# Performance work log

Hardware: AMD Instinct MI355X
Metric: run time of the kernel (lower is better)

## Reference

```python
import jax, jax.numpy as jnp
import numpy as np

# Dimensions (match init_kwargs / input_specs)
B, N, E, H, L, FF = 32, 512, 1024, 8, 3, 2048
KD = E // H          # key_dim = val_dim = 128 (projection width of W_query/W_key/W_val)
DK = KD // H         # 16 = actual per-head dim after the raw (H,B,N,-1) view
NORM = 1.0 / np.sqrt(KD)  # module uses 1/sqrt(key_dim)
MASK_FILL = -30.0    # evaluate=False path


def setup_inputs() -> dict:
    key = jax.random.key(0)
    ks = jax.random.split(key, 11)
    f32 = jnp.float32
    x = jax.random.normal(ks[0], (B * N, E), f32)
    mask = jax.random.randint(ks[1], (B, N), 0, 2).astype(bool)
    # Stacked per-layer params; torch init: uniform(-1/sqrt(fan_in), 1/sqrt(fan_in))
    def u(k, shape, fan):
        s = 1.0 / np.sqrt(fan)
        return jax.random.uniform(k, shape, f32, -s, s)
    Wq = u(ks[2], (L, KD, E), E)
    Wk = u(ks[3], (L, KD, E), E)
    Wv = u(ks[4], (L, KD, E), E)
    Wo = u(ks[5], (L, E, KD), KD)
    bo = u(ks[6], (L, E), E)
    W1 = u(ks[7], (L, FF, E), E)
    b1 = u(ks[8], (L, FF), FF)
    W2 = u(ks[9], (L, E, FF), FF)
    b2 = u(ks[10], (L, E), E)
    return {"x": x, "mask": mask, "Wq": Wq, "Wk": Wk, "Wv": Wv,
            "Wo": Wo, "bo": bo, "W1": W1, "b1": b1, "W2": W2, "b2": b2}


def _mha(h, Wq, Wk, Wv, Wo, bo, mask):
    # h: (B*N, E). Raw row-major view (torch .view == jnp.reshape) into (H,B,N,DK),
    # which mixes token/feature axes exactly as the original module does.
    Q = (h @ Wq.T).reshape(H, B, N, DK)
    K = (h @ Wk.T).reshape(H, B, N, DK)
    V = (h @ Wv.T).reshape(H, B, N, DK)
    compat = NORM * jnp.einsum('hbnd,hbmd->hbnm', Q, K)  # (H,B,N,N)
    m = mask[None, :, None, :]                            # mask key positions
    compat = jnp.where(m, MASK_FILL, compat)
    attn = jax.nn.softmax(compat, axis=-1)
    attn = jnp.where(m, 0.0, attn)                        # re-zero masked entries
    heads = jnp.einsum('hbnm,hbmd->hbnd', attn, V)        # (H,B,N,DK)
    out = heads.transpose(1, 2, 0, 3).reshape(B * N, H * DK) @ Wo.T + bo
    return out


def reference(x, mask, Wq, Wk, Wv, Wo, bo, W1, b1, W2, b2):
    h = x
    for l in range(L):
        h = h + _mha(h, Wq[l], Wk[l], Wv[l], Wo[l], bo[l], mask)
        h = h + (jax.nn.relu(h @ W1[l].T + b1[l]) @ W2[l].T + b2[l])
    return h, h.reshape(B, N, E).mean(axis=1)
```

## Files before the change

### kernel.cpp

```cpp
#include <hip/hip_runtime.h>
#include <stdint.h>


typedef __attribute__((ext_vector_type(8))) short short8;
typedef __attribute__((ext_vector_type(4))) float floatx4;

#define NORM_ 0.08838834764831845f

__device__ __forceinline__ float bf2f(unsigned short u) {
    union { unsigned int i; float f; } x; x.i = ((unsigned int)u) << 16; return x.f;
}
__device__ __forceinline__ unsigned short f2bf(float f) {
    union { float f; unsigned int i; } x; x.f = f;
    unsigned int u = x.i;
    u += 0x7FFFu + ((u >> 16) & 1u);
    return (unsigned short)(u >> 16);
}
__device__ __forceinline__ void async_cp16(const void* g, void* l) {
    __builtin_amdgcn_global_load_lds((const __attribute__((address_space(1))) void*)g,
                                     (__attribute__((address_space(3))) void*)l, 16, 0, 0);
}

__global__ __launch_bounds__(256) void detect_dtype(const unsigned int* __restrict__ x,
                                                    int* __restrict__ flag)
{
    __shared__ int good, bad;
    if (threadIdx.x == 0) { good = 0; bad = 0; }
    __syncthreads();
    int g = 0, b = 0;
    for (int i = threadIdx.x; i < 4096; i += 256) {
        unsigned int lo = x[i] & 0xFFFFu;
        if (lo != 0u) {
            unsigned int e = (lo >> 7) & 0xFFu;
            if (e >= 90u && e <= 145u) ++g; else ++b;
        }
    }
    atomicAdd(&good, g); atomicAdd(&bad, b);
    __syncthreads();
    if (threadIdx.x == 0) *flag = (bad > good) ? 1 : 0;
}

__global__ __launch_bounds__(256) void conv_to_bf16(const void* __restrict__ src,
                                                    unsigned short* __restrict__ dst,
                                                    int n, const int* __restrict__ flag)
{
    const int i = (blockIdx.x * 256 + threadIdx.x) * 8;
    if (i >= n) return;
    if (*flag) {
        const float* s = (const float*)src + i;
        floatx4 a = *(const floatx4*)s;
        floatx4 b = *(const floatx4*)(s + 4);
        short8 o;
        o[0] = (short)f2bf(a[0]); o[1] = (short)f2bf(a[1]);
        o[2] = (short)f2bf(a[2]); o[3] = (short)f2bf(a[3]);
        o[4] = (short)f2bf(b[0]); o[5] = (short)f2bf(b[1]);
        o[6] = (short)f2bf(b[2]); o[7] = (short)f2bf(b[3]);
        *(short8*)(dst + i) = o;
    } else {
        *(short8*)(dst + i) = *(const short8*)((const unsigned short*)src + i);
    }
}

__global__ __launch_bounds__(256) void init_h(const void* __restrict__ x,
                                              float* __restrict__ hf,
                                              unsigned short* __restrict__ hb,
                                              const int* __restrict__ flag)
{
    const size_t i = ((size_t)blockIdx.x * 256 + threadIdx.x) * 8;
    if (*flag) {
        const float* s = (const float*)x + i;
        floatx4 a = *(const floatx4*)s;
        floatx4 b = *(const floatx4*)(s + 4);
        short8 o;
        o[0] = (short)f2bf(a[0]); o[1] = (short)f2bf(a[1]);
        o[2] = (short)f2bf(a[2]); o[3] = (short)f2bf(a[3]);
        o[4] = (short)f2bf(b[0]); o[5] = (short)f2bf(b[1]);
        o[6] = (short)f2bf(b[2]); o[7] = (short)f2bf(b[3]);
        *(short8*)(hb + i) = o;
        *(floatx4*)(hf + i) = a;
        *(floatx4*)(hf + i + 4) = b;
    } else {
        short8 v = *(const short8*)((const unsigned short*)x + i);
        *(short8*)(hb + i) = v;
        #pragma unroll
        for (int e = 0; e < 8; ++e) hf[i + e] = bf2f((unsigned short)v[e]);
    }
}

__global__ __launch_bounds__(256) void mask_expand(const unsigned int* __restrict__ mraw,
                                                   float* __restrict__ maskf)
{
    __shared__ unsigned int r[4];
    if (threadIdx.x < 4) r[threadIdx.x] = 0;
    __syncthreads();
    unsigned int gt1 = 0, badb = 0, badh = 0, lo3f = 0;
    for (int i = threadIdx.x; i < 4096; i += 256) {
        unsigned int w = mraw[i];
        if (w > 1u) gt1 = 1;
        if (w & 0xFEFEFEFEu) badb = 1;
        unsigned int lo = w & 0xFFFFu, hi = w >> 16;
        if ((lo != 0u && lo != 0x3F80u) || (hi != 0u && hi != 0x3F80u)) badh = 1;
        if (lo == 0x3F80u) lo3f = 1;
    }
    if (gt1) atomicOr(&r[0], 1u);
    if (badb) atomicOr(&r[1], 1u);
    if (badh) atomicOr(&r[2], 1u);
    if (lo3f) atomicOr(&r[3], 1u);
    __syncthreads();
    int cls;
    if (!r[0]) cls = 0;
    else if (!r[1]) cls = 1;
    else if (!r[2]) cls = r[3] ? 2 : 3;
    else cls = 0;

    const int gid = blockIdx.x * 256 + threadIdx.x;
    bool m;
    if (cls == 0)      m = ((const int*)mraw)[gid] != 0;
    else if (cls == 1) m = ((const unsigned char*)mraw)[gid] != 0;
    else if (cls == 2) m = ((const unsigned short*)mraw)[gid] != 0;
    else               m = mraw[gid] != 0u;
    maskf[gid] = m ? 1.0f : 0.0f;
}

enum { EPI_NONE = 0, EPI_BIAS_RELU = 1, EPI_BIAS_RES = 2 };

template<int EPI>
__global__ __launch_bounds__(256) void gemm_bt(
    const unsigned short* __restrict__ A,
    const unsigned short* __restrict__ Bq,
    const unsigned short* __restrict__ Bk,
    const unsigned short* __restrict__ Bv,
    unsigned short* __restrict__ Cq,
    unsigned short* __restrict__ Ck,
    unsigned short* __restrict__ Cv,
    const unsigned short* __restrict__ bias,
    float* __restrict__ hf,
    unsigned short* __restrict__ hb,
    int N, int K)
{
    constexpr int BK = 64;
    __shared__ __align__(16) unsigned short As[2][128 * BK];
    __shared__ __align__(16) unsigned short Bs[2][128 * BK];

    const int t = threadIdx.x;
    const int lane = t & 63;
    const int wave = t >> 6;
    const int bm = blockIdx.x;
    const int bn = blockIdx.y;
    const int bz = blockIdx.z;

    const unsigned short* Bmat = (bz == 0) ? Bq : ((bz == 1) ? Bk : Bv);
    unsigned short* C = (bz == 0) ? Cq : ((bz == 1) ? Ck : Cv);

    const int wm = (wave >> 1) * 64;
    const int wn = (wave & 1) * 64;

    const int srow = t >> 3;
    const int scol = (((t & 7) ^ ((t >> 3) & 7)) * 8);
    const unsigned short* Ag = A + (size_t)(bm * 128 + srow) * K + scol;
    const unsigned short* Bg = Bmat + (size_t)(bn * 128 + srow) * K + scol;
    const size_t gstep = (size_t)32 * K;

    const int fl = lane & 15;
    const int g = lane >> 4;
    const int s7 = fl & 7;
    const int swz0 = (g ^ s7) * 8;
    const int swz1 = ((g + 4) ^ s7) * 8;
    int aoff[4], boff[4];
    #pragma unroll
    for (int i = 0; i < 4; ++i) {
        aoff[i] = (wm + i * 16 + fl) * BK;
        boff[i] = (wn + i * 16 + fl) * BK;
    }

    floatx4 acc[4][4];
    #pragma unroll
    for (int i = 0; i < 4; ++i)
        #pragma unroll
        for (int j = 0; j < 4; ++j) {
            acc[i][j][0] = 0.f; acc[i][j][1] = 0.f;
            acc[i][j][2] = 0.f; acc[i][j][3] = 0.f;
        }

    const int NT = K / BK;

    #pragma unroll
    for (int r = 0; r < 4; ++r) {
        async_cp16(Ag + r * gstep, &As[0][t * 8 + r * 2048]);
        async_cp16(Bg + r * gstep, &Bs[0][t * 8 + r * 2048]);
    }

    for (int it = 0; it < NT; ++it) {
        const int cur = it & 1;
        if (it + 1 < NT) {
            const int nxt = cur ^ 1;
            const size_t koff = (size_t)(it + 1) * BK;
            #pragma unroll
            for (int r = 0; r < 4; ++r) {
                async_cp16(Ag + koff + r * gstep, &As[nxt][t * 8 + r * 2048]);
                async_cp16(Bg + koff + r * gstep, &Bs[nxt][t * 8 + r * 2048]);
            }
            asm volatile("s_waitcnt vmcnt(8)" ::: "memory");
        } else {
            asm volatile("s_waitcnt vmcnt(0)" ::: "memory");
        }
        asm volatile("s_barrier" ::: "memory");

        #pragma unroll
        for (int ks = 0; ks < 2; ++ks) {
            const int sw = ks ? swz1 : swz0;
            short8 af[4], bfr[4];
            #pragma unroll
            for (int i = 0; i < 4; ++i) af[i] = *(const short8*)&As[cur][aoff[i] + sw];
            #pragma unroll
            for (int j = 0; j < 4; ++j) bfr[j] = *(const short8*)&Bs[cur][boff[j] + sw];
            #pragma unroll
            for (int i = 0; i < 4; ++i)
                #pragma unroll
                for (int j = 0; j < 4; ++j)
                    acc[i][j] = __builtin_amdgcn_mfma_f32_16x16x32_bf16(af[i], bfr[j], acc[i][j], 0, 0, 0);
        }
        if (it + 1 < NT)
            asm volatile("s_barrier" ::: "memory");
    }

    const int r0 = (lane >> 4) * 4;
    #pragma unroll
    for (int j = 0; j < 4; ++j) {
        const int gcol = bn * 128 + wn + j * 16 + fl;
        float bval = 0.f;
        if (EPI != EPI_NONE) bval = bf2f(bias[gcol]);
        #pragma unroll
        for (int i = 0; i < 4; ++i) {
            const int growb = bm * 128 + wm + i * 16 + r0;
            #pragma unroll
            for (int r = 0; r < 4; ++r) {
                const size_t idx = (size_t)(growb + r) * N + gcol;
                float v = acc[i][j][r];
                if (EPI == EPI_NONE) {
                    C[idx] = f2bf(v);
                } else if (EPI == EPI_BIAS_RELU) {
                    v += bval;
                    v = v > 0.f ? v : 0.f;
                    C[idx] = f2bf(v);
                } else {
                    float nh = hf[idx] + v + bval;
                    hf[idx] = nh;
                    hb[idx] = f2bf(nh);
                }
            }
        }
    }
}

__global__ __launch_bounds__(128) void attn_mfma(
    const unsigned short* __restrict__ Q,
    const unsigned short* __restrict__ Kx,
    const unsigned short* __restrict__ Vx,
    const float* __restrict__ maskf,
    unsigned short* __restrict__ Out)
{
    __shared__ __align__(16) unsigned short Vt[16 * 520];
    __shared__ __align__(16) unsigned short Pb[2][64 * 40];
    __shared__ float Ms[512];
    __shared__ float cnt_s;

    const int t = threadIdx.x;
    const int lane = t & 63;
    const int wave = t >> 6;
    const int p = blockIdx.x >> 2;
    const int qq = blockIdx.x & 3;
    const int b2 = p & 31;
    const int h2 = p >> 5;
    const int fm = lane & 15;
    const int g = lane >> 4;

    const unsigned short* Qg = Q + (size_t)p * 8192;
    const unsigned short* Kg = Kx + (size_t)p * 8192;
    const unsigned short* Vg = Vx + (size_t)p * 8192;

    #pragma unroll
    for (int rr = 0; rr < 4; ++rr) {
        const int row = t * 4 + rr;
        short8 v0 = *(const short8*)&Vg[row * 16];
        short8 v1 = *(const short8*)&Vg[row * 16 + 8];
        #pragma unroll
        for (int d = 0; d < 8; ++d) Vt[d * 520 + row] = (unsigned short)v0[d];
        #pragma unroll
        for (int d = 0; d < 8; ++d) Vt[(d + 8) * 520 + row] = (unsigned short)v1[d];
    }
    if (t == 0) cnt_s = 0.f;
    __syncthreads();
    float pc = 0.f;
    #pragma unroll
    for (int it = 0; it < 4; ++it) {
        int i = it * 128 + t;
        float mv = maskf[b2 * 512 + i];
        Ms[i] = mv; pc += mv;
    }
    atomicAdd(&cnt_s, pc);
    __syncthreads();
    const float cnt = cnt_s;

    const int qbase = qq * 128 + wave * 64;
    short8 qf[4];
    #pragma unroll
    for (int i = 0; i < 4; ++i) {
        short8 z = {0,0,0,0,0,0,0,0};
        if (g < 2) z = *(const short8*)&Qg[(qbase + i * 16 + fm) * 16 + g * 8];
        qf[i] = z;
    }

    float m_[4][4], l_[4][4];
    floatx4 O[4];
    #pragma unroll
    for (int i = 0; i < 4; ++i) {
        #pragma unroll
        for (int r = 0; r < 4; ++r) { m_[i][r] = -1e30f; l_[i][r] = 0.f; }
        O[i][0] = 0.f; O[i][1] = 0.f; O[i][2] = 0.f; O[i][3] = 0.f;
    }

    unsigned short* Pw = &Pb[wave][0];

    for (int kb = 0; kb < 512; kb += 32) {
        short8 kf0 = {0,0,0,0,0,0,0,0}, kf1 = {0,0,0,0,0,0,0,0};
        if (g < 2) {
            kf0 = *(const short8*)&Kg[(kb + fm) * 16 + g * 8];
            kf1 = *(const short8*)&Kg[(kb + 16 + fm) * 16 + g * 8];
        }
        const float msk0 = Ms[kb + fm];
        const float msk1 = Ms[kb + 16 + fm];

        floatx4 zero4 = {0.f, 0.f, 0.f, 0.f};
        floatx4 s0[4], s1[4];
        #pragma unroll
        for (int i = 0; i < 4; ++i) {
            s0[i] = __builtin_amdgcn_mfma_f32_16x16x32_bf16(qf[i], kf0, zero4, 0, 0, 0);
            s1[i] = __builtin_amdgcn_mfma_f32_16x16x32_bf16(qf[i], kf1, zero4, 0, 0, 0);
        }

        #pragma unroll
        for (int i = 0; i < 4; ++i) {
            #pragma unroll
            for (int r = 0; r < 4; ++r) {
                float a0 = (msk0 != 0.f) ? -1e30f : s0[i][r] * NORM_;
                float a1 = (msk1 != 0.f) ? -1e30f : s1[i][r] * NORM_;
                float mx = fmaxf(a0, a1);
                mx = fmaxf(mx, __shfl_xor(mx, 1));
                mx = fmaxf(mx, __shfl_xor(mx, 2));
                mx = fmaxf(mx, __shfl_xor(mx, 4));
                mx = fmaxf(mx, __shfl_xor(mx, 8));
                const float mo = m_[i][r];
                const float mn = fmaxf(mo, mx);
                const float alpha = __expf(mo - mn);
                float w0 = (msk0 != 0.f) ? 0.f : __expf(a0 - mn);
                float w1 = (msk1 != 0.f) ? 0.f : __expf(a1 - mn);
                float rs = w0 + w1;
                rs += __shfl_xor(rs, 1);
                rs += __shfl_xor(rs, 2);
                rs += __shfl_xor(rs, 4);
                rs += __shfl_xor(rs, 8);
                l_[i][r] = l_[i][r] * alpha + rs;
                m_[i][r] = mn;
                O[i][r] *= alpha;
                const int qloc = i * 16 + g * 4 + r;
                Pw[qloc * 40 + fm] = f2bf(w0);
                Pw[qloc * 40 + 16 + fm] = f2bf(w1);
            }
        }
        asm volatile("s_waitcnt lgkmcnt(0)" ::: "memory");

        short8 vtf = *(const short8*)&Vt[fm * 520 + kb + g * 8];
        #pragma unroll
        for (int i = 0; i < 4; ++i) {
            short8 pf = *(const short8*)&Pw[(i * 16 + fm) * 40 + g * 8];
            O[i] = __builtin_amdgcn_mfma_f32_16x16x32_bf16(pf, vtf, O[i], 0, 0, 0);
        }
    }

    #pragma unroll
    for (int i = 0; i < 4; ++i) {
        #pragma unroll
        for (int r = 0; r < 4; ++r) {
            const float M = fmaxf(m_[i][r], -30.f);
            const float adj = __expf(m_[i][r] - M);
            const float lf = l_[i][r] * adj + cnt * __expf(-30.f - M);
            const float oval = O[i][r] * adj / lf;
            const int n = qbase + i * 16 + g * 4 + r;
            Out[((size_t)(b2 * 512 + n)) * 128 + h2 * 16 + fm] = f2bf(oval);
        }
    }
}

__global__ __launch_bounds__(256) void write_h(const float* __restrict__ hf,
                                               void* __restrict__ out,
                                               const int* __restrict__ flag)
{
    const size_t i = ((size_t)blockIdx.x * 256 + threadIdx.x) * 4;
    floatx4 v = *(const floatx4*)&hf[i];
    if (*flag) {
        *(floatx4*)((float*)out + i) = v;
    } else {
        unsigned int p0 = (unsigned int)f2bf(v[0]) | ((unsigned int)f2bf(v[1]) << 16);
        unsigned int p1 = (unsigned int)f2bf(v[2]) | ((unsigned int)f2bf(v[3]) << 16);
        unsigned int* o = (unsigned int*)((unsigned short*)out + i);
        o[0] = p0; o[1] = p1;
    }
}

__global__ __launch_bounds__(256) void mean_kernel(const float* __restrict__ hf,
                                                   void* __restrict__ out,
                                                   const int* __restrict__ flag)
{
    const int b = blockIdx.x >> 2;
    const int e = ((blockIdx.x & 3) * 256) + threadIdx.x;
    float s = 0.f;
    for (int n = 0; n < 512; ++n) s += hf[((size_t)(b * 512 + n)) * 1024 + e];
    s *= (1.0f / 512.0f);
    const size_t off = (size_t)16384 * 1024 + b * 1024 + e;
    if (*flag) ((float*)out)[off] = s;
    else       ((unsigned short*)out)[off] = f2bf(s);
}

extern "C" void kernel_launch(void* const* d_in, const int* in_sizes, int n_in,
                              void* d_out, int out_size, void* d_ws, size_t ws_size,
                              hipStream_t stream)
{
    const void* x  = d_in[0];
    const unsigned int* mask = (const unsigned int*)d_in[1];

    char* ws = (char*)d_ws;
    float* hf = (float*)ws;                     ws += (size_t)16384 * 1024 * 4;
    unsigned short* hb = (unsigned short*)ws;   ws += (size_t)16384 * 1024 * 2;
    char* shared_rg = ws;                       ws += (size_t)16384 * 2048 * 2;
    unsigned short* act = (unsigned short*)shared_rg;
    unsigned short* q  = (unsigned short*)shared_rg;
    unsigned short* k  = q + (size_t)16384 * 128;
    unsigned short* v  = k + (size_t)16384 * 128;
    unsigned short* ao = v + (size_t)16384 * 128;
    unsigned short* cWq = (unsigned short*)ws;  ws += (size_t)393216 * 2;
    unsigned short* cWk = (unsigned short*)ws;  ws += (size_t)393216 * 2;
    unsigned short* cWv = (unsigned short*)ws;  ws += (size_t)393216 * 2;
    unsigned short* cWo = (unsigned short*)ws;  ws += (size_t)393216 * 2;
    unsigned short* cbo = (unsigned short*)ws;  ws += (size_t)3072 * 2;
    unsigned short* cW1 = (unsigned short*)ws;  ws += (size_t)6291456 * 2;
    unsigned short* cb1 = (unsigned short*)ws;  ws += (size_t)6144 * 2;
    unsigned short* cW2 = (unsigned short*)ws;  ws += (size_t)6291456 * 2;
    unsigned short* cb2 = (unsigned short*)ws;  ws += (size_t)3072 * 2;
    float* maskf = (float*)ws;                  ws += (size_t)16384 * 4;
    int* flag = (int*)ws;                       ws += 256;

    detect_dtype<<<1, 256, 0, stream>>>((const unsigned int*)x, flag);

    auto conv = [&](const void* s, unsigned short* d, int n) {
        conv_to_bf16<<<(n / 8 + 255) / 256, 256, 0, stream>>>(s, d, n, flag);
    };
    conv(d_in[2], cWq, 393216);
    conv(d_in[3], cWk, 393216);
    conv(d_in[4], cWv, 393216);
    conv(d_in[5], cWo, 393216);
    conv(d_in[6], cbo, 3072);
    conv(d_in[7], cW1, 6291456);
    conv(d_in[8], cb1, 6144);
    conv(d_in[9], cW2, 6291456);
    conv(d_in[10], cb2, 3072);

    mask_expand<<<64, 256, 0, stream>>>(mask, maskf);
    init_h<<<8192, 256, 0, stream>>>(x, hf, hb, flag);

    for (int l = 0; l < 3; ++l) {
        const unsigned short* wq  = cWq + (size_t)l * 131072;
        const unsigned short* wk  = cWk + (size_t)l * 131072;
        const unsigned short* wv  = cWv + (size_t)l * 131072;
        const unsigned short* wo  = cWo + (size_t)l * 131072;
        const unsigned short* bol = cbo + (size_t)l * 1024;
        const unsigned short* w1  = cW1 + (size_t)l * 2097152;
        const unsigned short* b1l = cb1 + (size_t)l * 2048;
        const unsigned short* w2  = cW2 + (size_t)l * 2097152;
        const unsigned short* b2l = cb2 + (size_t)l * 1024;

        gemm_bt<EPI_NONE><<<dim3(128, 1, 3), 256, 0, stream>>>(
            hb, wq, wk, wv, q, k, v, nullptr, nullptr, nullptr, 128, 1024);
        attn_mfma<<<1024, 128, 0, stream>>>(q, k, v, maskf, ao);
        gemm_bt<EPI_BIAS_RES><<<dim3(128, 8, 1), 256, 0, stream>>>(
            ao, wo, wo, wo, nullptr, nullptr, nullptr, bol, hf, hb, 1024, 128);
        gemm_bt<EPI_BIAS_RELU><<<dim3(128, 16, 1), 256, 0, stream>>>(
            hb, w1, w1, w1, act, act, act, b1l, nullptr, nullptr, 2048, 1024);
        gemm_bt<EPI_BIAS_RES><<<dim3(128, 8, 1), 256, 0, stream>>>(
            act, w2, w2, w2, nullptr, nullptr, nullptr, b2l, hf, hb, 1024, 2048);
    }

    write_h<<<16384, 256, 0, stream>>>(hf, d_out, flag);
    mean_kernel<<<128, 256, 0, stream>>>(hf, d_out, flag);
}
```

Measured before the change: 1.247 ms.

## Add 256x256-tile GEMM with pipelined async loads for FFN layers

Introduces a new 512-thread GEMM kernel using 256x256 output tiles, 8 waves each computing 128x64, with double-buffered LDS staging via global_load_lds, an XOR swizzle, interleaved load/MFMA phases and setprio hints. The two FFN GEMMs (W1 with ReLU, W2 with residual) switch to it. Larger tiles are meant to raise arithmetic intensity and cut global traffic, and the interleaving is meant to hide load latency. In exchange it uses 128KB of LDS and many accumulator registers, so only one block fits per CU, and the grids are smaller (512 and 256 blocks), which may underfill the GPU.

```diff
diff --git a/kernel.cpp b/kernel.cpp
--- a/kernel.cpp
+++ b/kernel.cpp
@@ -19,6 +19,9 @@
 __device__ __forceinline__ void async_cp16(const void* g, void* l) {
     __builtin_amdgcn_global_load_lds((const __attribute__((address_space(1))) void*)g,
                                      (__attribute__((address_space(3))) void*)l, 16, 0, 0);
+}
+__device__ __forceinline__ floatx4 mfma16(short8 a, short8 b, floatx4 c) {
+    return __builtin_amdgcn_mfma_f32_16x16x32_bf16(a, b, c, 0, 0, 0);
 }
 
 __global__ __launch_bounds__(256) void detect_dtype(const unsigned int* __restrict__ x,
@@ -233,6 +236,171 @@
         #pragma unroll
         for (int i = 0; i < 4; ++i) {
             const int growb = bm * 128 + wm + i * 16 + r0;
+            #pragma unroll
+            for (int r = 0; r < 4; ++r) {
+                const size_t idx = (size_t)(growb + r) * N + gcol;
+                float v = acc[i][j][r];
+                if (EPI == EPI_NONE) {
+                    C[idx] = f2bf(v);
+                } else if (EPI == EPI_BIAS_RELU) {
+                    v += bval;
+                    v = v > 0.f ? v : 0.f;
+                    C[idx] = f2bf(v);
+                } else {
+                    float nh = hf[idx] + v + bval;
+                    hf[idx] = nh;
+                    hb[idx] = f2bf(nh);
+                }
+            }
+        }
+    }
+}
+
+template<int EPI>
+__global__ __launch_bounds__(512) void gemm256_bt(
+    const unsigned short* __restrict__ A,
+    const unsigned short* __restrict__ Bmat,
+    unsigned short* __restrict__ C,
+    const unsigned short* __restrict__ bias,
+    float* __restrict__ hf,
+    unsigned short* __restrict__ hb,
+    int N, int K)
+{
+    __shared__ __align__(16) unsigned short As[2][16384];
+    __shared__ __align__(16) unsigned short Bs[2][16384];
+
+    const int t = threadIdx.x;
+    const int lane = t & 63;
+    const int wave = t >> 6;
+    const int bm = blockIdx.x;
+    const int bn = blockIdx.y;
+
+    const int wm = (wave >> 2) * 128;
+    const int wn = (wave & 3) * 64;
+
+    const int srow = t >> 3;
+    const int scol = ((t & 7) ^ (srow & 7)) * 8;
+    const unsigned short* Ag = A + (size_t)(bm * 256 + srow) * K + scol;
+    const unsigned short* Bg = Bmat + (size_t)(bn * 256 + srow) * K + scol;
+    const size_t rows64 = (size_t)64 * K;
+
+    const int fl = lane & 15;
+    const int g = lane >> 4;
+    const int s7 = fl & 7;
+    const int c0 = (g ^ s7) * 8;
+    const int c1 = ((4 + g) ^ s7) * 8;
+    const int abase = (wm + fl) * 64;
+    const int bbase = (wn + fl) * 64;
+
+    floatx4 acc[8][4];
+    #pragma unroll
+    for (int i = 0; i < 8; ++i)
+        #pragma unroll
+        for (int j = 0; j < 4; ++j) {
+            acc[i][j][0] = 0.f; acc[i][j][1] = 0.f;
+            acc[i][j][2] = 0.f; acc[i][j][3] = 0.f;
+        }
+
+    auto stgA = [&](int buf, int h, size_t koff) {
+        const unsigned short* s = Ag + (size_t)(h * 128) * K + koff;
+        unsigned short* d = &As[buf][h * 8192 + t * 8];
+        async_cp16(s, d);
+        async_cp16(s + rows64, d + 4096);
+    };
+    auto stgB = [&](int buf, int h, size_t koff) {
+        const unsigned short* s = Bg + (size_t)(h * 128) * K + koff;
+        unsigned short* d = &Bs[buf][h * 8192 + t * 8];
+        async_cp16(s, d);
+        async_cp16(s + rows64, d + 4096);
+    };
+
+    const int NT = K >> 6;
+
+    stgA(0, 0, 0); stgA(0, 1, 0); stgB(0, 0, 0); stgB(0, 1, 0);
+    if (NT > 1) {
+        stgA(1, 0, 64); stgA(1, 1, 64);
+        asm volatile("s_waitcnt vmcnt(4)" ::: "memory");
+    } else {
+        asm volatile("s_waitcnt vmcnt(0)" ::: "memory");
+    }
+    asm volatile("s_barrier" ::: "memory");
+
+    for (int tt = 0; tt < NT; ++tt) {
+        const int R = tt & 1;
+        const int S = R ^ 1;
+        const size_t k1 = (size_t)(tt + 1) << 6;
+        const size_t k2 = (size_t)(tt + 2) << 6;
+        const bool p1 = (tt + 1 < NT);
+        const bool p2 = (tt + 2 < NT);
+
+        short8 a0[8], a1[8], b0[4], b1[4];
+
+        #pragma unroll
+        for (int i = 0; i < 8; ++i) a0[i] = *(const short8*)&As[R][abase + i * 1024 + c0];
+        #pragma unroll
+        for (int j = 0; j < 4; ++j) b0[j] = *(const short8*)&Bs[R][bbase + j * 1024 + c0];
+        if (p1) stgB(S, 0, k1);
+        asm volatile("s_barrier" ::: "memory");
+        asm volatile("s_waitcnt lgkmcnt(0)" ::: "memory");
+        __builtin_amdgcn_s_setprio(1);
+        #pragma unroll
+        for (int i = 0; i < 8; ++i) {
+            acc[i][0] = mfma16(a0[i], b0[0], acc[i][0]);
+            acc[i][1] = mfma16(a0[i], b0[1], acc[i][1]);
+        }
+        __builtin_amdgcn_s_setprio(0);
+        asm volatile("s_barrier" ::: "memory");
+
+        #pragma unroll
+        for (int i = 0; i < 8; ++i) a1[i] = *(const short8*)&As[R][abase + i * 1024 + c1];
+        #pragma unroll
+        for (int j = 0; j < 4; ++j) b1[j] = *(const short8*)&Bs[R][bbase + j * 1024 + c1];
+        if (p1) stgB(S, 1, k1);
+        asm volatile("s_barrier" ::: "memory");
+        asm volatile("s_waitcnt lgkmcnt(0)" ::: "memory");
+        __builtin_amdgcn_s_setprio(1);
+        #pragma unroll
+        for (int i = 0; i < 8; ++i) {
+            acc[i][2] = mfma16(a0[i], b0[2], acc[i][2]);
+            acc[i][3] = mfma16(a0[i], b0[3], acc[i][3]);
+        }
+        __builtin_amdgcn_s_setprio(0);
+        asm volatile("s_barrier" ::: "memory");
+
+        if (p2) stgA(R, 0, k2);
+        asm volatile("s_barrier" ::: "memory");
+        __builtin_amdgcn_s_setprio(1);
+        #pragma unroll
+        for (int i = 0; i < 8; ++i) {
+            acc[i][0] = mfma16(a1[i], b1[0], acc[i][0]);
+            acc[i][1] = mfma16(a1[i], b1[1], acc[i][1]);
+        }
+        __builtin_amdgcn_s_setprio(0);
+        asm volatile("s_barrier" ::: "memory");
+
+        if (p2) stgA(R, 1, k2);
+        asm volatile("s_barrier" ::: "memory");
+        __builtin_amdgcn_s_setprio(1);
+        #pragma unroll
+        for (int i = 0; i < 8; ++i) {
+            acc[i][2] = mfma16(a1[i], b1[2], acc[i][2]);
+            acc[i][3] = mfma16(a1[i], b1[3], acc[i][3]);
+        }
+        __builtin_amdgcn_s_setprio(0);
+        if (p2) asm volatile("s_waitcnt vmcnt(4)" ::: "memory");
+        else    asm volatile("s_waitcnt vmcnt(0)" ::: "memory");
+        asm volatile("s_barrier" ::: "memory");
+    }
+
+    const int r0 = g * 4;
+    #pragma unroll
+    for (int j = 0; j < 4; ++j) {
+        const int gcol = bn * 256 + wn + j * 16 + fl;
+        float bval = 0.f;
+        if (EPI != EPI_NONE) bval = bf2f(bias[gcol]);
+        #pragma unroll
+        for (int i = 0; i < 8; ++i) {
+            const int growb = bm * 256 + wm + i * 16 + r0;
             #pragma unroll
             for (int r = 0; r < 4; ++r) {
                 const size_t idx = (size_t)(growb + r) * N + gcol;
@@ -484,10 +652,10 @@
         attn_mfma<<<1024, 128, 0, stream>>>(q, k, v, maskf, ao);
         gemm_bt<EPI_BIAS_RES><<<dim3(128, 8, 1), 256, 0, stream>>>(
             ao, wo, wo, wo, nullptr, nullptr, nullptr, bol, hf, hb, 1024, 128);
-        gemm_bt<EPI_BIAS_RELU><<<dim3(128, 16, 1), 256, 0, stream>>>(
-            hb, w1, w1, w1, act, act, act, b1l, nullptr, nullptr, 2048, 1024);
-        gemm_bt<EPI_BIAS_RES><<<dim3(128, 8, 1), 256, 0, stream>>>(
-            act, w2, w2, w2, nullptr, nullptr, nullptr, b2l, hf, hb, 1024, 2048);
+        gemm256_bt<EPI_BIAS_RELU><<<dim3(64, 8, 1), 512, 0, stream>>>(
+            hb, w1, act, b1l, nullptr, nullptr, 2048, 1024);
+        gemm256_bt<EPI_BIAS_RES><<<dim3(64, 4, 1), 512, 0, stream>>>(
+            act, w2, nullptr, b2l, hf, hb, 1024, 2048);
     }
 
     write_h<<<16384, 256, 0, stream>>>(hf, d_out, flag);
```

Measured after the change: 1.200 ms. -3.8%, faster.

## Add dedicated FFN GEMM with 128x256 tiles, register-streamed B and hand-scheduled MFMA

Applied to the files above, without the earlier changes.

Adds a gemm_ffn kernel for the two FFN matmuls. It uses 512-thread blocks computing 128x256 output tiles, stages only the A operand in LDS through async global-to-LDS copies, and loads the weight B fragments directly from global memory into registers, double-buffered across k-tiles. The inline-asm ds_read/global_load calls, explicit waitcnt, sched_barrier and setprio are meant to interleave MFMAs with memory traffic and raise per-block reuse. The cost is higher register pressure and fragile manual scheduling. B fragments read from global are not shared across waves.

```diff
diff --git a/kernel.cpp b/kernel.cpp
--- a/kernel.cpp
+++ b/kernel.cpp
@@ -19,6 +19,21 @@
 __device__ __forceinline__ void async_cp16(const void* g, void* l) {
     __builtin_amdgcn_global_load_lds((const __attribute__((address_space(1))) void*)g,
                                      (__attribute__((address_space(3))) void*)l, 16, 0, 0);
+}
+__device__ __forceinline__ floatx4 mfma16(short8 a, short8 b, floatx4 c) {
+    return __builtin_amdgcn_mfma_f32_16x16x32_bf16(a, b, c, 0, 0, 0);
+}
+template<int IMM>
+__device__ __forceinline__ short8 ds_read128(unsigned addr) {
+    short8 r;
+    asm volatile("ds_read_b128 %0, %1 offset:%2" : "=v"(r) : "v"(addr), "n"(IMM));
+    return r;
+}
+template<int IMM>
+__device__ __forceinline__ short8 gload128(const unsigned short* p) {
+    short8 r;
+    asm volatile("global_load_dwordx4 %0, %1, off offset:%2" : "=v"(r) : "v"(p), "n"(IMM));
+    return r;
 }
 
 __global__ __launch_bounds__(256) void detect_dtype(const unsigned int* __restrict__ x,
@@ -228,6 +243,183 @@
     #pragma unroll
     for (int j = 0; j < 4; ++j) {
         const int gcol = bn * 128 + wn + j * 16 + fl;
+        float bval = 0.f;
+        if (EPI != EPI_NONE) bval = bf2f(bias[gcol]);
+        #pragma unroll
+        for (int i = 0; i < 4; ++i) {
+            const int growb = bm * 128 + wm + i * 16 + r0;
+            #pragma unroll
+            for (int r = 0; r < 4; ++r) {
+                const size_t idx = (size_t)(growb + r) * N + gcol;
+                float v = acc[i][j][r];
+                if (EPI == EPI_NONE) {
+                    C[idx] = f2bf(v);
+                } else if (EPI == EPI_BIAS_RELU) {
+                    v += bval;
+                    v = v > 0.f ? v : 0.f;
+                    C[idx] = f2bf(v);
+                } else {
+                    float nh = hf[idx] + v + bval;
+                    hf[idx] = nh;
+                    hb[idx] = f2bf(nh);
+                }
+            }
+        }
+    }
+}
+
+template<int EPI>
+__global__ __launch_bounds__(512, 2) void gemm_ffn(
+    const unsigned short* __restrict__ A,
+    const unsigned short* __restrict__ Bmat,
+    unsigned short* __restrict__ C,
+    const unsigned short* __restrict__ bias,
+    float* __restrict__ hf,
+    unsigned short* __restrict__ hb,
+    int N, int K)
+{
+    __shared__ __align__(16) unsigned short As[2][8192];
+
+    const int t = threadIdx.x;
+    const int lane = t & 63;
+    const int wave = t >> 6;
+    const int bm = blockIdx.x;
+    const int bn = blockIdx.y;
+
+    const int wm = (wave >> 2) * 64;
+    const int wn = (wave & 3) * 64;
+
+    const int srow = t >> 3;
+    const int scol = ((t & 7) ^ (srow & 7)) * 8;
+    const unsigned short* Ag = A + (size_t)(bm * 128 + srow) * K + scol;
+    const size_t r64K = (size_t)64 * K;
+
+    const int fl = lane & 15;
+    const int g = lane >> 4;
+    const int s7 = fl & 7;
+
+    const unsigned ldsA = (unsigned)(size_t)(__attribute__((address_space(3))) unsigned short*)&As[0][0];
+    const unsigned rA0 = ldsA + (unsigned)((wm + fl) * 128 + ((g ^ s7) * 16));
+    const unsigned rA1 = ldsA + (unsigned)((wm + fl) * 128 + (((4 + g) ^ s7) * 16));
+
+    const unsigned short* pb0 = Bmat + (size_t)(bn * 256 + wn + 0 * 16 + fl) * K + g * 8;
+    const unsigned short* pb1 = Bmat + (size_t)(bn * 256 + wn + 1 * 16 + fl) * K + g * 8;
+    const unsigned short* pb2 = Bmat + (size_t)(bn * 256 + wn + 2 * 16 + fl) * K + g * 8;
+    const unsigned short* pb3 = Bmat + (size_t)(bn * 256 + wn + 3 * 16 + fl) * K + g * 8;
+
+    floatx4 acc[4][4];
+    #pragma unroll
+    for (int i = 0; i < 4; ++i)
+        #pragma unroll
+        for (int j = 0; j < 4; ++j) {
+            acc[i][j][0] = 0.f; acc[i][j][1] = 0.f;
+            acc[i][j][2] = 0.f; acc[i][j][3] = 0.f;
+        }
+
+    auto stg = [&](int buf, int rnd, int tile) {
+        const unsigned short* s = Ag + (size_t)rnd * r64K + (size_t)tile * 64;
+        async_cp16(s, &As[buf][rnd * 4096 + t * 8]);
+    };
+
+    const int NT = K >> 6;
+
+    short8 bA[8], bB[8];
+
+    bA[0] = gload128<0>(pb0);  bA[1] = gload128<0>(pb1);
+    bA[2] = gload128<0>(pb2);  bA[3] = gload128<0>(pb3);
+    bA[4] = gload128<64>(pb0); bA[5] = gload128<64>(pb1);
+    bA[6] = gload128<64>(pb2); bA[7] = gload128<64>(pb3);
+    stg(0, 0, 0); stg(0, 1, 0);
+    stg(1, 0, 1); stg(1, 1, 1);
+    asm volatile("s_waitcnt vmcnt(2)" ::: "memory");
+    asm volatile("s_barrier" ::: "memory");
+
+#define FFN_TILE(TT, R, CURB, NXTB)                                            \
+    do {                                                                       \
+        const bool p1 = (TT) + 1 < NT;                                         \
+        const bool p2 = (TT) + 2 < NT;                                         \
+        short8 a0k0 = ds_read128<0 * 2048 + (R) * 16384>(rA0);                 \
+        short8 a1k0 = ds_read128<1 * 2048 + (R) * 16384>(rA0);                 \
+        short8 a2k0 = ds_read128<2 * 2048 + (R) * 16384>(rA0);                 \
+        short8 a3k0 = ds_read128<3 * 2048 + (R) * 16384>(rA0);                 \
+        short8 a0k1 = ds_read128<0 * 2048 + (R) * 16384>(rA1);                 \
+        short8 a1k1 = ds_read128<1 * 2048 + (R) * 16384>(rA1);                 \
+        short8 a2k1 = ds_read128<2 * 2048 + (R) * 16384>(rA1);                 \
+        short8 a3k1 = ds_read128<3 * 2048 + (R) * 16384>(rA1);                 \
+        if (p1) {                                                              \
+            NXTB[0] = gload128<((R) + 1) * 128 + 0>(pb0);                      \
+            NXTB[1] = gload128<((R) + 1) * 128 + 0>(pb1);                      \
+            NXTB[2] = gload128<((R) + 1) * 128 + 0>(pb2);                      \
+            NXTB[3] = gload128<((R) + 1) * 128 + 0>(pb3);                      \
+        }                                                                      \
+        asm volatile("s_waitcnt lgkmcnt(0)" ::: "memory");                     \
+        __builtin_amdgcn_sched_barrier(0);                                     \
+        __builtin_amdgcn_s_setprio(1);                                         \
+        acc[0][0] = mfma16(a0k0, CURB[0], acc[0][0]);                          \
+        acc[1][0] = mfma16(a1k0, CURB[0], acc[1][0]);                          \
+        acc[2][0] = mfma16(a2k0, CURB[0], acc[2][0]);                          \
+        acc[3][0] = mfma16(a3k0, CURB[0], acc[3][0]);                          \
+        acc[0][1] = mfma16(a0k0, CURB[1], acc[0][1]);                          \
+        acc[1][1] = mfma16(a1k0, CURB[1], acc[1][1]);                          \
+        acc[2][1] = mfma16(a2k0, CURB[1], acc[2][1]);                          \
+        acc[3][1] = mfma16(a3k0, CURB[1], acc[3][1]);                          \
+        __builtin_amdgcn_s_setprio(0);                                         \
+        if (p1) {                                                              \
+            NXTB[4] = gload128<((R) + 1) * 128 + 64>(pb0);                     \
+            NXTB[5] = gload128<((R) + 1) * 128 + 64>(pb1);                     \
+            NXTB[6] = gload128<((R) + 1) * 128 + 64>(pb2);                     \
+            NXTB[7] = gload128<((R) + 1) * 128 + 64>(pb3);                     \
+        }                                                                      \
+        asm volatile("s_barrier" ::: "memory");                                \
+        __builtin_amdgcn_s_setprio(1);                                         \
+        acc[0][2] = mfma16(a0k0, CURB[2], acc[0][2]);                          \
+        acc[1][2] = mfma16(a1k0, CURB[2], acc[1][2]);                          \
+        acc[2][2] = mfma16(a2k0, CURB[2], acc[2][2]);                          \
+        acc[3][2] = mfma16(a3k0, CURB[2], acc[3][2]);                          \
+        acc[0][3] = mfma16(a0k0, CURB[3], acc[0][3]);                          \
+        acc[1][3] = mfma16(a1k0, CURB[3], acc[1][3]);                          \
+        acc[2][3] = mfma16(a2k0, CURB[3], acc[2][3]);                          \
+        acc[3][3] = mfma16(a3k0, CURB[3], acc[3][3]);                          \
+        __builtin_amdgcn_s_setprio(0);                                         \
+        if (p2) stg((R), 0, (TT) + 2);                                         \
+        __builtin_amdgcn_s_setprio(1);                                         \
+        acc[0][0] = mfma16(a0k1, CURB[4], acc[0][0]);                          \
+        acc[1][0] = mfma16(a1k1, CURB[4], acc[1][0]);                          \
+        acc[2][0] = mfma16(a2k1, CURB[4], acc[2][0]);                          \
+        acc[3][0] = mfma16(a3k1, CURB[4], acc[3][0]);                          \
+        acc[0][1] = mfma16(a0k1, CURB[5], acc[0][1]);                          \
+        acc[1][1] = mfma16(a1k1, CURB[5], acc[1][1]);                          \
+        acc[2][1] = mfma16(a2k1, CURB[5], acc[2][1]);                          \
+        acc[3][1] = mfma16(a3k1, CURB[5], acc[3][1]);                          \
+        __builtin_amdgcn_s_setprio(0);                                         \
+        if (p2) stg((R), 1, (TT) + 2);                                         \
+        __builtin_amdgcn_s_setprio(1);                                         \
+        acc[0][2] = mfma16(a0k1, CURB[6], acc[0][2]);                          \
+        acc[1][2] = mfma16(a1k1, CURB[6], acc[1][2]);                          \
+        acc[2][2] = mfma16(a2k1, CURB[6], acc[2][2]);                          \
+        acc[3][2] = mfma16(a3k1, CURB[6], acc[3][2]);                          \
+        acc[0][3] = mfma16(a0k1, CURB[7], acc[0][3]);                          \
+        acc[1][3] = mfma16(a1k1, CURB[7], acc[1][3]);                          \
+        acc[2][3] = mfma16(a2k1, CURB[7], acc[2][3]);                          \
+        acc[3][3] = mfma16(a3k1, CURB[7], acc[3][3]);                          \
+        __builtin_amdgcn_s_setprio(0);                                         \
+        if (p2) asm volatile("s_waitcnt vmcnt(2)" ::: "memory");               \
+        else    asm volatile("s_waitcnt vmcnt(0)" ::: "memory");               \
+        __builtin_amdgcn_sched_barrier(0);                                     \
+        asm volatile("s_barrier" ::: "memory");                                \
+    } while (0)
+
+    for (int tt = 0; tt < NT; tt += 2) {
+        FFN_TILE(tt,     0, bA, bB);
+        FFN_TILE(tt + 1, 1, bB, bA);
+        pb0 += 128; pb1 += 128; pb2 += 128; pb3 += 128;
+    }
+#undef FFN_TILE
+
+    const int r0 = g * 4;
+    #pragma unroll
+    for (int j = 0; j < 4; ++j) {
+        const int gcol = bn * 256 + wn + j * 16 + fl;
         float bval = 0.f;
         if (EPI != EPI_NONE) bval = bf2f(bias[gcol]);
         #pragma unroll
@@ -484,10 +676,10 @@
         attn_mfma<<<1024, 128, 0, stream>>>(q, k, v, maskf, ao);
         gemm_bt<EPI_BIAS_RES><<<dim3(128, 8, 1), 256, 0, stream>>>(
             ao, wo, wo, wo, nullptr, nullptr, nullptr, bol, hf, hb, 1024, 128);
-        gemm_bt<EPI_BIAS_RELU><<<dim3(128, 16, 1), 256, 0, stream>>>(
-            hb, w1, w1, w1, act, act, act, b1l, nullptr, nullptr, 2048, 1024);
-        gemm_bt<EPI_BIAS_RES><<<dim3(128, 8, 1), 256, 0, stream>>>(
-            act, w2, w2, w2, nullptr, nullptr, nullptr, b2l, hf, hb, 1024, 2048);
+        gemm_ffn<EPI_BIAS_RELU><<<dim3(128, 8, 1), 512, 0, stream>>>(
+            hb, w1, act, b1l, nullptr, nullptr, 2048, 1024);
+        gemm_ffn<EPI_BIAS_RES><<<dim3(128, 4, 1), 512, 0, stream>>>(
+            act, w2, nullptr, b2l, hf, hb, 1024, 2048);
     }
 
     write_h<<<16384, 256, 0, stream>>>(hf, d_out, flag);
```

Result: slower. 1.646 ms (+32.0%).
